# Optimization experiments

Hardware: AMD Instinct MI355X
Metric: run time of the kernel (lower is better)

The kernel has to match this reference:

```python
import jax, jax.numpy as jnp
import numpy as np

N = 100000   # nodes
E = 1600000  # edges (avg degree 16)
D_IN, D_HID, D_OUT = 128, 128, 64
BN_EPS = 1e-5


def setup_inputs() -> dict:
    key = jax.random.key(0)
    ks = jax.random.split(key, 12)
    nf_mat = jax.random.normal(ks[0], (N, D_IN), dtype=jnp.float32)
    edge_index = jax.random.randint(ks[1], (2, E), 0, N, dtype=jnp.int32)
    # pre-normalized adjacency weights (GCNConv normalize=True is folded into conv_mat here)
    edge_weight = jax.random.uniform(ks[2], (E,), dtype=jnp.float32) * (1.0 / 16.0)
    def glorot(k, fan_in, fan_out):
        s = jnp.sqrt(6.0 / (fan_in + fan_out)).astype(jnp.float32)
        return jax.random.uniform(k, (fan_in, fan_out), dtype=jnp.float32, minval=-s, maxval=s)
    return {
        "nf_mat": nf_mat,
        "edge_index": edge_index,
        "edge_weight": edge_weight,
        "W0": glorot(ks[3], D_IN, D_HID), "b0": jnp.zeros((D_HID,), jnp.float32),
        "W1": glorot(ks[4], D_HID, D_HID), "b1": jnp.zeros((D_HID,), jnp.float32),
        "W2": glorot(ks[5], D_HID, D_OUT), "b2": jnp.zeros((D_OUT,), jnp.float32),
        "gamma0": jnp.ones((D_HID,), jnp.float32), "beta0": jnp.zeros((D_HID,), jnp.float32),
        "gamma1": jnp.ones((D_HID,), jnp.float32), "beta1": jnp.zeros((D_HID,), jnp.float32),
    }


def _gcn_conv(x, W, b, src, dst, w):
    # GCNConv: aggregate A_norm @ (x W) + b over the sparse edge list
    h = x @ W                                   # [N, F_out]
    msg = h[src] * w[:, None]                   # [E, F_out] gather + scale
    agg = jax.ops.segment_sum(msg, dst, num_segments=N)  # scatter-add -> [N, F_out]
    return agg + b


def _batchnorm(x, gamma, beta):
    # BatchNorm1d over node dimension (training-mode batch statistics, biased var)
    mu = jnp.mean(x, axis=0)
    var = jnp.mean(jnp.square(x - mu), axis=0)
    return gamma * (x - mu) * jax.lax.rsqrt(var + BN_EPS) + beta


def reference(nf_mat, edge_index, edge_weight, W0, b0, W1, b1, W2, b2,
              gamma0, beta0, gamma1, beta1):
    src, dst = edge_index[0], edge_index[1]
    x = nf_mat
    # layer 0: conv -> BN -> ReLU (dropout is identity in eval)
    x = _gcn_conv(x, W0, b0, src, dst, edge_weight)
    x = jax.nn.relu(_batchnorm(x, gamma0, beta0))
    # layer 1
    x = _gcn_conv(x, W1, b1, src, dst, edge_weight)
    x = jax.nn.relu(_batchnorm(x, gamma1, beta1))
    # final conv, then cross-node sum
    x = _gcn_conv(x, W2, b2, src, dst, edge_weight)
    return jnp.sum(x, axis=0)  # [D_OUT]
```

## Files before the change

kernel.cpp:

```cpp
#include <hip/hip_runtime.h>

#define BN_EPS 1e-5f

#define NPB 512
#define NPB_SHIFT 9
#define PB 512
#define MAXB 256
#define WCB 200
#define WCCAP 16
#define NSLICE 16

typedef __attribute__((ext_vector_type(8))) short short8;
typedef __attribute__((ext_vector_type(4))) float floatx4;
typedef __attribute__((ext_vector_type(2))) float floatx2;

__device__ __forceinline__ unsigned short f2bf(float f) {
    unsigned u = __float_as_uint(f);
    unsigned r = u + 0x7FFFu + ((u >> 16) & 1u);
    return (unsigned short)(r >> 16);
}
__device__ __forceinline__ float blo(unsigned v) { return __uint_as_float(v << 16); }
__device__ __forceinline__ float bhi(unsigned v) { return __uint_as_float(v & 0xffff0000u); }

__device__ __forceinline__ uint2 pk8_fp8(const float4 v0, const float4 v1) {
    int lo = 0, hi = 0;
    lo = __builtin_amdgcn_cvt_pk_fp8_f32(v0.x, v0.y, lo, false);
    lo = __builtin_amdgcn_cvt_pk_fp8_f32(v0.z, v0.w, lo, true);
    hi = __builtin_amdgcn_cvt_pk_fp8_f32(v1.x, v1.y, hi, false);
    hi = __builtin_amdgcn_cvt_pk_fp8_f32(v1.z, v1.w, hi, true);
    return make_uint2((unsigned)lo, (unsigned)hi);
}

__global__ __launch_bounds__(256) void wconv(
    const float* __restrict__ W0, const float* __restrict__ W1,
    unsigned short* __restrict__ wt0, unsigned short* __restrict__ wt1,
    float* __restrict__ stats)
{
    const int idx = blockIdx.x * 256 + threadIdx.x;
    const int n = idx >> 7, k = idx & 127;
    wt0[idx] = f2bf(W0[k * 128 + n]);
    wt1[idx] = f2bf(W1[k * 128 + n]);
    if (blockIdx.x < 10) {
        const int o = (blockIdx.x * 256 + threadIdx.x) * 4;
        *(float4*)&stats[o] = make_float4(0.f, 0.f, 0.f, 0.f);
    }
}

__global__ __launch_bounds__(256) void gemm0(
    const float* __restrict__ A, const unsigned short* __restrict__ Wt,
    uint2* __restrict__ C, int M)
{
    __shared__ char lds[53248];
    unsigned short* Al = (unsigned short*)lds;
    unsigned short* Wl = (unsigned short*)(lds + 17408);
    float* Cl = (float*)lds;

    const int tid = threadIdx.x;
    const int r0 = blockIdx.x * 64;

#pragma unroll
    for (int i = 0; i < 16; ++i) {
        const int idx = i * 256 + tid;
        const int n = idx >> 5, q = idx & 31;
        const ushort4 v = ((const ushort4*)Wt)[idx];
        *(ushort4*)&Wl[n * 136 + q * 4] = v;
    }
#pragma unroll
    for (int i = 0; i < 8; ++i) {
        const int row = i * 8 + (tid >> 5), q = tid & 31;
        const int gr = r0 + row;
        float4 v = (gr < M) ? ((const float4*)A)[(size_t)gr * 32 + q]
                            : make_float4(0.f, 0.f, 0.f, 0.f);
        ushort4 o;
        o.x = f2bf(v.x); o.y = f2bf(v.y); o.z = f2bf(v.z); o.w = f2bf(v.w);
        *(ushort4*)&Al[row * 136 + q * 4] = o;
    }
    __syncthreads();

    const int wave = tid >> 6, lane = tid & 63;
    const int lrow = lane & 15, quad = lane >> 4;
    const int n0 = wave * 32;

    floatx4 acc[4][2];
#pragma unroll
    for (int mt = 0; mt < 4; ++mt)
#pragma unroll
        for (int t = 0; t < 2; ++t)
#pragma unroll
            for (int j = 0; j < 4; ++j) acc[mt][t][j] = 0.f;

#pragma unroll
    for (int c = 0; c < 4; ++c) {
        const int k0 = c * 32;
        const short8 b0 = *(const short8*)&Wl[(n0 + lrow) * 136 + k0 + quad * 8];
        const short8 b1 = *(const short8*)&Wl[(n0 + 16 + lrow) * 136 + k0 + quad * 8];
#pragma unroll
        for (int mt = 0; mt < 4; ++mt) {
            const short8 a = *(const short8*)&Al[(mt * 16 + lrow) * 136 + k0 + quad * 8];
            acc[mt][0] = __builtin_amdgcn_mfma_f32_16x16x32_bf16(a, b0, acc[mt][0], 0, 0, 0);
            acc[mt][1] = __builtin_amdgcn_mfma_f32_16x16x32_bf16(a, b1, acc[mt][1], 0, 0, 0);
        }
    }
    __syncthreads();

#pragma unroll
    for (int mt = 0; mt < 4; ++mt)
#pragma unroll
        for (int t = 0; t < 2; ++t)
#pragma unroll
            for (int j = 0; j < 4; ++j)
                Cl[(mt * 16 + quad * 4 + j) * 132 + n0 + t * 16 + lrow] = acc[mt][t][j];
    __syncthreads();

#pragma unroll
    for (int i = 0; i < 4; ++i) {
        const int row = i * 16 + (tid >> 4);
        const int c0 = (tid & 15) * 8;
        const int gr = r0 + row;
        if (gr < M) {
            const float4 v0 = *(float4*)&Cl[row * 132 + c0];
            const float4 v1 = *(float4*)&Cl[row * 132 + c0 + 4];
            C[(size_t)gr * 16 + (c0 >> 3)] = pk8_fp8(v0, v1);
        }
    }
}

__global__ __launch_bounds__(256) void gemm1(
    const unsigned* __restrict__ Ab, const unsigned short* __restrict__ Wt,
    uint2* __restrict__ C,
    const float* __restrict__ sum, const float* __restrict__ sq,
    const float* __restrict__ g, const float* __restrict__ be,
    int M, int N)
{
    __shared__ char lds[53248];
    unsigned short* Al = (unsigned short*)lds;
    unsigned short* Wl = (unsigned short*)(lds + 17408);
    float* AscL = (float*)(lds + 52224);
    float* AshL = AscL + 128;
    float* Cl = (float*)lds;

    const int tid = threadIdx.x;
    const int r0 = blockIdx.x * 64;

    if (tid < 128) {
        float s = 0.f, q = 0.f;
#pragma unroll
        for (int k = 0; k < NSLICE; ++k) {
            s += sum[k * 128 + tid];
            q += sq[k * 128 + tid];
        }
        const float invN = 1.0f / (float)N;
        const float m = s * invN;
        const float var = q * invN - m * m;
        const float rs = rsqrtf(var + BN_EPS);
        AscL[tid] = g[tid] * rs;
        AshL[tid] = be[tid] - g[tid] * m * rs;
    }
    __syncthreads();

#pragma unroll
    for (int i = 0; i < 16; ++i) {
        const int idx = i * 256 + tid;
        const int n = idx >> 5, q = idx & 31;
        const ushort4 v = ((const ushort4*)Wt)[idx];
        *(ushort4*)&Wl[n * 136 + q * 4] = v;
    }
#pragma unroll
    for (int i = 0; i < 4; ++i) {
        const int idx = i * 256 + tid;
        const int row = idx >> 4, qc = idx & 15;
        const int gr = r0 + row;
        uint4 v = (gr < M) ? ((const uint4*)Ab)[(size_t)gr * 16 + qc]
                           : make_uint4(0, 0, 0, 0);
        const float4 a0 = *(const float4*)&AscL[qc * 8];
        const float4 a1 = *(const float4*)&AscL[qc * 8 + 4];
        const float4 b0 = *(const float4*)&AshL[qc * 8];
        const float4 b1 = *(const float4*)&AshL[qc * 8 + 4];
        float x0 = fmaxf(fmaf(a0.x, blo(v.x), b0.x), 0.f);
        float x1 = fmaxf(fmaf(a0.y, bhi(v.x), b0.y), 0.f);
        float x2 = fmaxf(fmaf(a0.z, blo(v.y), b0.z), 0.f);
        float x3 = fmaxf(fmaf(a0.w, bhi(v.y), b0.w), 0.f);
        float x4 = fmaxf(fmaf(a1.x, blo(v.z), b1.x), 0.f);
        float x5 = fmaxf(fmaf(a1.y, bhi(v.z), b1.y), 0.f);
        float x6 = fmaxf(fmaf(a1.z, blo(v.w), b1.z), 0.f);
        float x7 = fmaxf(fmaf(a1.w, bhi(v.w), b1.w), 0.f);
        uint4 o;
        o.x = (unsigned)f2bf(x0) | ((unsigned)f2bf(x1) << 16);
        o.y = (unsigned)f2bf(x2) | ((unsigned)f2bf(x3) << 16);
        o.z = (unsigned)f2bf(x4) | ((unsigned)f2bf(x5) << 16);
        o.w = (unsigned)f2bf(x6) | ((unsigned)f2bf(x7) << 16);
        *(uint4*)&Al[row * 136 + qc * 8] = o;
    }
    __syncthreads();

    const int wave = tid >> 6, lane = tid & 63;
    const int lrow = lane & 15, quad = lane >> 4;
    const int n0 = wave * 32;

    floatx4 acc[4][2];
#pragma unroll
    for (int mt = 0; mt < 4; ++mt)
#pragma unroll
        for (int t = 0; t < 2; ++t)
#pragma unroll
            for (int j = 0; j < 4; ++j) acc[mt][t][j] = 0.f;

#pragma unroll
    for (int c = 0; c < 4; ++c) {
        const int k0 = c * 32;
        const short8 b0 = *(const short8*)&Wl[(n0 + lrow) * 136 + k0 + quad * 8];
        const short8 b1 = *(const short8*)&Wl[(n0 + 16 + lrow) * 136 + k0 + quad * 8];
#pragma unroll
        for (int mt = 0; mt < 4; ++mt) {
            const short8 a = *(const short8*)&Al[(mt * 16 + lrow) * 136 + k0 + quad * 8];
            acc[mt][0] = __builtin_amdgcn_mfma_f32_16x16x32_bf16(a, b0, acc[mt][0], 0, 0, 0);
            acc[mt][1] = __builtin_amdgcn_mfma_f32_16x16x32_bf16(a, b1, acc[mt][1], 0, 0, 0);
        }
    }
    __syncthreads();

#pragma unroll
    for (int mt = 0; mt < 4; ++mt)
#pragma unroll
        for (int t = 0; t < 2; ++t)
#pragma unroll
            for (int j = 0; j < 4; ++j)
                Cl[(mt * 16 + quad * 4 + j) * 132 + n0 + t * 16 + lrow] = acc[mt][t][j];
    __syncthreads();

#pragma unroll
    for (int i = 0; i < 4; ++i) {
        const int row = i * 16 + (tid >> 4);
        const int c0 = (tid & 15) * 8;
        const int gr = r0 + row;
        if (gr < M) {
            const float4 v0 = *(float4*)&Cl[row * 132 + c0];
            const float4 v1 = *(float4*)&Cl[row * 132 + c0 + 4];
            C[(size_t)gr * 16 + (c0 >> 3)] = pk8_fp8(v0, v1);
        }
    }
}


__global__ __launch_bounds__(512) void bucket_hist(
    const int* __restrict__ src, const int* __restrict__ dst,
    int* __restrict__ cntD, int* __restrict__ cntS, int E, int B, int chunk)
{
    __shared__ int hD[MAXB], hS[MAXB];
    const int tid = threadIdx.x;
    for (int i = tid; i < B; i += 512) { hD[i] = 0; hS[i] = 0; }
    __syncthreads();
    const int lo = blockIdx.x * chunk;
    const int hi = min(E, lo + chunk);
    for (int e = lo + tid; e < hi; e += 512) {
        atomicAdd(&hD[dst[e] >> NPB_SHIFT], 1);
        atomicAdd(&hS[src[e] >> NPB_SHIFT], 1);
    }
    __syncthreads();
    for (int i = tid; i < B; i += 512) {
        cntD[i * PB + blockIdx.x] = hD[i];
        cntS[i * PB + blockIdx.x] = hS[i];
    }
}

__global__ __launch_bounds__(256) void bucket_base(
    const int* __restrict__ cntD, const int* __restrict__ cntS,
    int* __restrict__ baseD, int* __restrict__ baseS, int B, int E)
{
    __shared__ int lD[256], lS[256];
    const int tid = threadIdx.x;
    int sD = 0, sS = 0;
    if (tid < B) {
        const int4* pD = (const int4*)(cntD + tid * PB);
        const int4* pS = (const int4*)(cntS + tid * PB);
        for (int j = 0; j < PB / 4; ++j) {
            const int4 a = pD[j], b = pS[j];
            sD += a.x + a.y + a.z + a.w;
            sS += b.x + b.y + b.z + b.w;
        }
    }
    lD[tid] = sD; lS[tid] = sS;
    __syncthreads();
    for (int st = 1; st < 256; st <<= 1) {
        const int vD = (tid >= st) ? lD[tid - st] : 0;
        const int vS = (tid >= st) ? lS[tid - st] : 0;
        __syncthreads();
        lD[tid] += vD; lS[tid] += vS;
        __syncthreads();
    }
    if (tid < B) { baseD[tid] = lD[tid] - sD; baseS[tid] = lS[tid] - sS; }
    if (tid == 0) { baseD[B] = E; baseS[B] = E; }
}

__global__ __launch_bounds__(256) void bucket_cursor(
    int* __restrict__ cntD, int* __restrict__ cntS,
    const int* __restrict__ baseD, const int* __restrict__ baseS, int B)
{
    int b = blockIdx.x;
    int* cnt; const int* base;
    if (b < B) { cnt = cntD; base = baseD; }
    else       { cnt = cntS; base = baseS; b -= B; }
    __shared__ int ls[256];
    const int tid = threadIdx.x;
    const int c0 = cnt[b * PB + 2 * tid];
    const int c1 = cnt[b * PB + 2 * tid + 1];
    const int s = c0 + c1;
    ls[tid] = s;
    __syncthreads();
    for (int st = 1; st < 256; st <<= 1) {
        const int v = (tid >= st) ? ls[tid - st] : 0;
        __syncthreads();
        ls[tid] += v;
        __syncthreads();
    }
    const int excl = ls[tid] - s + base[b];
    cnt[b * PB + 2 * tid] = excl;
    cnt[b * PB + 2 * tid + 1] = excl + c0;
}

__global__ __launch_bounds__(512) void bucket_place(
    const int* __restrict__ src, const int* __restrict__ dst,
    const float* __restrict__ ew,
    const int* __restrict__ curD, const int* __restrict__ curS,
    uint2* __restrict__ bktD, uint2* __restrict__ bktS, int E, int B, int chunk)
{
    __shared__ uint2 bufD[WCB][WCCAP + 1], bufS[WCB][WCCAP + 1];
    __shared__ int tailD[WCB], tailS[WCB], gcurD[WCB], gcurS[WCB];
    const int tid = threadIdx.x;
    for (int i = tid; i < B; i += 512) {
        gcurD[i] = curD[i * PB + blockIdx.x];
        gcurS[i] = curS[i * PB + blockIdx.x];
        tailD[i] = 0; tailS[i] = 0;
    }
    __syncthreads();
    const int lo = blockIdx.x * chunk;
    const int hi = min(E, lo + chunk);
    const int nt = (hi - lo + 511) >> 9;
    for (int t = 0; t < nt; ++t) {
        const int e = lo + t * 512 + tid;
        if (e < hi) {
            const int s = src[e], d = dst[e];
            const unsigned wb = __float_as_uint(ew[e]);
            const int bd = d >> NPB_SHIFT;
            const uint2 rd = make_uint2(((unsigned)s << NPB_SHIFT) | (unsigned)(d & (NPB - 1)), wb);
            const int pd = atomicAdd(&tailD[bd], 1);
            if (pd < WCCAP) bufD[bd][pd] = rd;
            else            bktD[gcurD[bd] + pd] = rd;
            const int bs = s >> NPB_SHIFT;
            const uint2 rs = make_uint2((unsigned)(s & (NPB - 1)), wb);
            const int ps = atomicAdd(&tailS[bs], 1);
            if (ps < WCCAP) bufS[bs][ps] = rs;
            else            bktS[gcurS[bs] + ps] = rs;
        }
        __syncthreads();
        const bool last = (t == nt - 1);
        if (tid < B) {
            {
                const int tl = tailD[tid];
                const int nb = min(tl, WCCAP);
                const int k = last ? nb : (nb & ~7);
                const int base = gcurD[tid];
                for (int i = 0; i < k; ++i) bktD[base + i] = bufD[tid][i];
                const int adv = (tl > WCCAP) ? tl : k;
                const int left = (tl > WCCAP) ? 0 : (tl - k);
                for (int i = 0; i < left; ++i) bufD[tid][i] = bufD[tid][k + i];
                gcurD[tid] = base + adv;
                tailD[tid] = left;
            }
            {
                const int tl = tailS[tid];
                const int nb = min(tl, WCCAP);
                const int k = last ? nb : (nb & ~7);
                const int base = gcurS[tid];
                for (int i = 0; i < k; ++i) bktS[base + i] = bufS[tid][i];
                const int adv = (tl > WCCAP) ? tl : k;
                const int left = (tl > WCCAP) ? 0 : (tl - k);
                for (int i = 0; i < left; ++i) bufS[tid][i] = bufS[tid][k + i];
                gcurS[tid] = base + adv;
                tailS[tid] = left;
            }
        }
        __syncthreads();
    }
}

__global__ __launch_bounds__(256) void bucket_sortcw(
    const uint2* __restrict__ bktD, const int* __restrict__ baseD,
    int* __restrict__ rp, int2* __restrict__ packed,
    const uint2* __restrict__ bktS, const int* __restrict__ baseS,
    float* __restrict__ cw, int N, int B)
{
    const int tid = threadIdx.x;
    if (blockIdx.x >= B) {
        const int b = blockIdx.x - B;
        const int lo = baseS[b], hi = baseS[b + 1];
        __shared__ float sm[NPB];
        sm[2 * tid] = 0.f; sm[2 * tid + 1] = 0.f;
        __syncthreads();
        for (int i = lo + tid; i < hi; i += 256) {
            const uint2 r = bktS[i];
            atomicAdd(&sm[r.x], __uint_as_float(r.y));
        }
        __syncthreads();
        const int n0 = b * NPB + 2 * tid;
        if (n0 < N)     cw[n0]     = sm[2 * tid];
        if (n0 + 1 < N) cw[n0 + 1] = sm[2 * tid + 1];
        return;
    }
    const int b = blockIdx.x;
    const int lo = baseD[b], hi = baseD[b + 1];
    __shared__ int cnt[NPB], cur[NPB];
    __shared__ int ls[256];
    cnt[2 * tid] = 0; cnt[2 * tid + 1] = 0;
    __syncthreads();
    for (int i = lo + tid; i < hi; i += 256)
        atomicAdd(&cnt[bktD[i].x & (NPB - 1)], 1);
    __syncthreads();
    const int c0 = cnt[2 * tid], c1 = cnt[2 * tid + 1];
    const int s = c0 + c1;
    ls[tid] = s;
    __syncthreads();
    for (int st = 1; st < 256; st <<= 1) {
        const int v = (tid >= st) ? ls[tid - st] : 0;
        __syncthreads();
        ls[tid] += v;
        __syncthreads();
    }
    const int excl = ls[tid] - s;
    const int n0 = b * NPB + 2 * tid;
    if (n0 < N)     rp[n0]     = lo + excl + c0;
    if (n0 + 1 < N) rp[n0 + 1] = lo + excl + c0 + c1;
    cur[2 * tid]     = lo + excl;
    cur[2 * tid + 1] = lo + excl + c0;
    __syncthreads();
    for (int i = lo + tid; i < hi; i += 256) {
        const uint2 r = bktD[i];
        const int pos = atomicAdd(&cur[r.x & (NPB - 1)], 1);
        packed[pos] = make_int2((int)(r.x >> NPB_SHIFT) << 4, (int)r.y);
    }
}


#define ACC_EDGE(V, W, A) do { \
    floatx2 w2_; w2_.x = (W); w2_.y = (W); \
    floatx2 f_; \
    f_ = __builtin_amdgcn_cvt_pk_f32_fp8((int)(V).x, false); \
    A[0] = f_ * w2_ + A[0]; \
    f_ = __builtin_amdgcn_cvt_pk_f32_fp8((int)(V).x, true);  \
    A[1] = f_ * w2_ + A[1]; \
    f_ = __builtin_amdgcn_cvt_pk_f32_fp8((int)(V).y, false); \
    A[2] = f_ * w2_ + A[2]; \
    f_ = __builtin_amdgcn_cvt_pk_f32_fp8((int)(V).y, true);  \
    A[3] = f_ * w2_ + A[3]; \
} while (0)

__global__ __launch_bounds__(256) void aggq(
    const int2* __restrict__ packed, const int* __restrict__ rp,
    const uint2* __restrict__ h2, uint4* __restrict__ aggb4,
    float* __restrict__ sum, float* __restrict__ sq, int N)
{
    __shared__ int2 eb[16][65];
    __shared__ float lsum[512], lsq[512];

    const int tid = threadIdx.x;
    const int lane = tid & 63, wave = tid >> 6;
    const int sub = lane >> 4;
    const int u = lane & 15;
    const int wq = wave * 4 + sub;
    const int nb0 = blockIdx.x * 32;
    const int nX = nb0 + wq * 2, nY = nX + 1;
    int2* ebq = eb[wq];

    int rpv = 0;
    {
        const int idx = nb0 - 1 + lane;
        if (lane <= 32 && idx >= 0 && idx < N) rpv = rp[idx];
    }
    const int sX = __shfl(rpv, 2 * wq, 64);
    const int eX = __shfl(rpv, 2 * wq + 1, 64);
    const int eYr = __shfl(rpv, 2 * wq + 2, 64);
    const int sY = eX;
    const int dXf = max(eX - sX, 0), dYf = max(eYr - sY, 0);
    const int eXe = sX + dXf, eYe = sY + dYf;

    {
        int2 r;
        r = (u      < dXf) ? packed[sX + u]      : make_int2(0, 0); ebq[u]      = r;
        r = (u + 16 < dXf) ? packed[sX + 16 + u] : make_int2(0, 0); ebq[16 + u] = r;
        r = (u      < dYf) ? packed[sY + u]      : make_int2(0, 0); ebq[32 + u] = r;
        r = (u + 16 < dYf) ? packed[sY + 16 + u] : make_int2(0, 0); ebq[48 + u] = r;
    }

    floatx2 aX[4], aY[4];
#pragma unroll
    for (int k = 0; k < 4; ++k) { aX[k] = 0.f; aY[k] = 0.f; }

    const int cX = min(dXf, 32), cY = min(dYf, 32);
    const int jmax = (cX > cY) ? cX : cY;

    for (int j = 0; j < jmax; j += 4) {
        const int2 x0 = ebq[j],      x1 = ebq[j + 1];
        const int2 x2 = ebq[j + 2],  x3 = ebq[j + 3];
        const int2 y0 = ebq[32 + j],     y1 = ebq[32 + j + 1];
        const int2 y2 = ebq[32 + j + 2], y3 = ebq[32 + j + 3];
        const uint2 vx0 = h2[(size_t)(unsigned)(x0.x + u)];
        const uint2 vx1 = h2[(size_t)(unsigned)(x1.x + u)];
        const uint2 vx2 = h2[(size_t)(unsigned)(x2.x + u)];
        const uint2 vx3 = h2[(size_t)(unsigned)(x3.x + u)];
        const uint2 vy0 = h2[(size_t)(unsigned)(y0.x + u)];
        const uint2 vy1 = h2[(size_t)(unsigned)(y1.x + u)];
        const uint2 vy2 = h2[(size_t)(unsigned)(y2.x + u)];
        const uint2 vy3 = h2[(size_t)(unsigned)(y3.x + u)];
        ACC_EDGE(vx0, __int_as_float(x0.y), aX);
        ACC_EDGE(vx1, __int_as_float(x1.y), aX);
        ACC_EDGE(vx2, __int_as_float(x2.y), aX);
        ACC_EDGE(vx3, __int_as_float(x3.y), aX);
        ACC_EDGE(vy0, __int_as_float(y0.y), aY);
        ACC_EDGE(vy1, __int_as_float(y1.y), aY);
        ACC_EDGE(vy2, __int_as_float(y2.y), aY);
        ACC_EDGE(vy3, __int_as_float(y3.y), aY);
    }

    for (int base = sX + 32; base < eXe; base += 32) {
        const int rem = eXe - base;
        int2 r;
        r = (u      < rem) ? packed[base + u]      : make_int2(0, 0); ebq[u]      = r;
        r = (u + 16 < rem) ? packed[base + 16 + u] : make_int2(0, 0); ebq[16 + u] = r;
        const int cc = min(rem, 32);
        for (int j = 0; j < cc; j += 4) {
            const int2 x0 = ebq[j], x1 = ebq[j + 1], x2 = ebq[j + 2], x3 = ebq[j + 3];
            const uint2 v0 = h2[(size_t)(unsigned)(x0.x + u)];
            const uint2 v1 = h2[(size_t)(unsigned)(x1.x + u)];
            const uint2 v2 = h2[(size_t)(unsigned)(x2.x + u)];
            const uint2 v3 = h2[(size_t)(unsigned)(x3.x + u)];
            ACC_EDGE(v0, __int_as_float(x0.y), aX);
            ACC_EDGE(v1, __int_as_float(x1.y), aX);
            ACC_EDGE(v2, __int_as_float(x2.y), aX);
            ACC_EDGE(v3, __int_as_float(x3.y), aX);
        }
    }
    for (int base = sY + 32; base < eYe; base += 32) {
        const int rem = eYe - base;
        int2 r;
        r = (u      < rem) ? packed[base + u]      : make_int2(0, 0); ebq[32 + u] = r;
        r = (u + 16 < rem) ? packed[base + 16 + u] : make_int2(0, 0); ebq[48 + u] = r;
        const int cc = min(rem, 32);
        for (int j = 0; j < cc; j += 4) {
            const int2 y0 = ebq[32 + j], y1 = ebq[32 + j + 1];
            const int2 y2 = ebq[32 + j + 2], y3 = ebq[32 + j + 3];
            const uint2 v0 = h2[(size_t)(unsigned)(y0.x + u)];
            const uint2 v1 = h2[(size_t)(unsigned)(y1.x + u)];
            const uint2 v2 = h2[(size_t)(unsigned)(y2.x + u)];
            const uint2 v3 = h2[(size_t)(unsigned)(y3.x + u)];
            ACC_EDGE(v0, __int_as_float(y0.y), aY);
            ACC_EDGE(v1, __int_as_float(y1.y), aY);
            ACC_EDGE(v2, __int_as_float(y2.y), aY);
            ACC_EDGE(v3, __int_as_float(y3.y), aY);
        }
    }

    if (nX < N) {
        uint4 o;
        o.x = (unsigned)f2bf(aX[0].x) | ((unsigned)f2bf(aX[0].y) << 16);
        o.y = (unsigned)f2bf(aX[1].x) | ((unsigned)f2bf(aX[1].y) << 16);
        o.z = (unsigned)f2bf(aX[2].x) | ((unsigned)f2bf(aX[2].y) << 16);
        o.w = (unsigned)f2bf(aX[3].x) | ((unsigned)f2bf(aX[3].y) << 16);
        aggb4[(size_t)nX * 16 + u] = o;
    }
    if (nY < N) {
        uint4 o;
        o.x = (unsigned)f2bf(aY[0].x) | ((unsigned)f2bf(aY[0].y) << 16);
        o.y = (unsigned)f2bf(aY[1].x) | ((unsigned)f2bf(aY[1].y) << 16);
        o.z = (unsigned)f2bf(aY[2].x) | ((unsigned)f2bf(aY[2].y) << 16);
        o.w = (unsigned)f2bf(aY[3].x) | ((unsigned)f2bf(aY[3].y) << 16);
        aggb4[(size_t)nY * 16 + u] = o;
    }

    floatx2 cs0 = aX[0] + aY[0], cs1 = aX[1] + aY[1];
    floatx2 cs2 = aX[2] + aY[2], cs3 = aX[3] + aY[3];
    floatx2 cq0 = aX[0] * aX[0] + aY[0] * aY[0];
    floatx2 cq1 = aX[1] * aX[1] + aY[1] * aY[1];
    floatx2 cq2 = aX[2] * aX[2] + aY[2] * aY[2];
    floatx2 cq3 = aX[3] * aX[3] + aY[3] * aY[3];
#define XRED(V) \
    V.x += __shfl_xor(V.x, 16, 64); V.y += __shfl_xor(V.y, 16, 64); \
    V.x += __shfl_xor(V.x, 32, 64); V.y += __shfl_xor(V.y, 32, 64);
    XRED(cs0) XRED(cs1) XRED(cs2) XRED(cs3)
    XRED(cq0) XRED(cq1) XRED(cq2) XRED(cq3)
#undef XRED
    const floatx2 ws = (sub == 0) ? cs0 : (sub == 1) ? cs1 : (sub == 2) ? cs2 : cs3;
    const floatx2 wwq = (sub == 0) ? cq0 : (sub == 1) ? cq1 : (sub == 2) ? cq2 : cq3;
    const int col = u * 8 + 2 * sub;
    lsum[wave * 128 + col] = ws.x;  lsum[wave * 128 + col + 1] = ws.y;
    lsq[wave * 128 + col]  = wwq.x; lsq[wave * 128 + col + 1]  = wwq.y;
    __syncthreads();
    if (tid < 128) {
        float s = 0.f, q = 0.f;
#pragma unroll
        for (int i = 0; i < 4; ++i) {
            s += lsum[i * 128 + tid];
            q += lsq[i * 128 + tid];
        }
        const int sl = (blockIdx.x & (NSLICE - 1)) * 128;
        atomicAdd(&sum[sl + tid], s);
        atomicAdd(&sq[sl + tid], q);
    }
}

__global__ __launch_bounds__(256) void wcolsum_bf16(
    const uint2* __restrict__ xb2, const float* __restrict__ cw,
    const float* __restrict__ sum1, const float* __restrict__ sq1,
    const float* __restrict__ g, const float* __restrict__ be,
    float* __restrict__ sout, int N)
{
    __shared__ float Aaf[128], Baf[128];
    __shared__ float4 ls[256];
    const int tid = threadIdx.x;
    if (tid < 128) {
        float s = 0.f, q = 0.f;
#pragma unroll
        for (int k = 0; k < NSLICE; ++k) {
            s += sum1[k * 128 + tid];
            q += sq1[k * 128 + tid];
        }
        const float invN = 1.0f / (float)N;
        const float m = s * invN;
        const float var = q * invN - m * m;
        const float rs = rsqrtf(var + BN_EPS);
        Aaf[tid] = g[tid] * rs;
        Baf[tid] = be[tid] - g[tid] * m * rs;
    }
    __syncthreads();
    const int u2 = tid & 31;
    const int half = (tid >> 5) & 1;
    const int rr = tid >> 6;
    const float4 A = *(const float4*)&Aaf[u2 * 4];
    const float4 Bv = *(const float4*)&Baf[u2 * 4];
    float4 s = make_float4(0.f, 0.f, 0.f, 0.f);
    for (int row = blockIdx.x * 8 + rr * 2 + half; row < N; row += gridDim.x * 8) {
        const uint2 v = xb2[(size_t)row * 32 + u2];
        const float c = cw[row];
        s.x = fmaf(c, fmaxf(fmaf(A.x, blo(v.x), Bv.x), 0.f), s.x);
        s.y = fmaf(c, fmaxf(fmaf(A.y, bhi(v.x), Bv.y), 0.f), s.y);
        s.z = fmaf(c, fmaxf(fmaf(A.z, blo(v.y), Bv.z), 0.f), s.z);
        s.w = fmaf(c, fmaxf(fmaf(A.w, bhi(v.y), Bv.w), 0.f), s.w);
    }
    ls[tid] = s;
    __syncthreads();
    if (tid < 32) {
        float4 a = ls[tid];
#pragma unroll
        for (int k = 1; k < 8; ++k) {
            const float4 b = ls[tid + 32 * k];
            a.x += b.x; a.y += b.y; a.z += b.z; a.w += b.w;
        }
        float* so = sout + (blockIdx.x & (NSLICE - 1)) * 128 + tid * 4;
        atomicAdd(&so[0], a.x);
        atomicAdd(&so[1], a.y);
        atomicAdd(&so[2], a.z);
        atomicAdd(&so[3], a.w);
    }
}

__global__ void final_out(
    const float* __restrict__ s, const float* __restrict__ W2,
    const float* __restrict__ b2, float* __restrict__ out, int N, int Dout)
{
    __shared__ float sv[128];
    const int j = threadIdx.x;
    {
        float a = 0.f;
#pragma unroll
        for (int k = 0; k < NSLICE; ++k) a += s[k * 128 + j];
        sv[j] = a;
    }
    __syncthreads();
    if (j < Dout) {
        float acc = 0.f;
        for (int f = 0; f < 128; ++f) acc = fmaf(sv[f], W2[f * Dout + j], acc);
        out[j] = acc + (float)N * b2[j];
    }
}

extern "C" void kernel_launch(void* const* d_in, const int* in_sizes, int n_in,
                              void* d_out, int out_size, void* d_ws, size_t ws_size,
                              hipStream_t stream)
{
    const float* nf  = (const float*)d_in[0];
    const int*   ei  = (const int*)d_in[1];
    const float* ew  = (const float*)d_in[2];
    const float* W0  = (const float*)d_in[3];
    const float* W1  = (const float*)d_in[5];
    const float* W2  = (const float*)d_in[7];
    const float* b2  = (const float*)d_in[8];
    const float* g0  = (const float*)d_in[9];
    const float* be0 = (const float*)d_in[10];
    const float* g1  = (const float*)d_in[11];
    const float* be1 = (const float*)d_in[12];

    const int N = in_sizes[0] / 128;
    const int E = in_sizes[2];
    const int* srcI = ei;
    const int* dstI = ei + E;

    const int B = (N + NPB - 1) / NPB;
    const int chunk = (E + PB - 1) / PB;

    const size_t HB = ((size_t)N * 128 * 2 + 255) & ~(size_t)255;
    const size_t NA = ((size_t)N * sizeof(int) + 255) & ~(size_t)255;
    const size_t CB = (((size_t)B * PB * 4) + 255) & ~(size_t)255;
    char* ws = (char*)d_ws;
    size_t off = 0;
    float* cw    = (float*)(ws + off); off += NA;
    int*   rp    = (int*)  (ws + off); off += NA;
    float* stats = (float*)(ws + off); off += 40960;
    int*   cntD  = (int*)  (ws + off); off += CB;
    int*   cntS  = (int*)  (ws + off); off += CB;
    int*   baseD = (int*)  (ws + off); off += 2048;
    int*   baseS = (int*)  (ws + off); off += 2048;
    uint2* hbuf  = (uint2*)(ws + off); off += HB;
    unsigned* aggb = (unsigned*)(ws + off); off += HB;
    int2*  packed = (int2*)(ws + off); off += (size_t)E * 8;
    uint2* bktD  = (uint2*)(ws + off); off += (size_t)E * 8;
    uint2* bktS  = (uint2*)(ws + off); off += (size_t)E * 8;
    unsigned short* wt0 = (unsigned short*)(ws + off); off += 32768;
    unsigned short* wt1 = (unsigned short*)(ws + off); off += 32768;
    (void)ws_size;

    float* sum0 = stats + 0 * NSLICE * 128;
    float* sq0  = stats + 1 * NSLICE * 128;
    float* sum1 = stats + 2 * NSLICE * 128;
    float* sq1  = stats + 3 * NSLICE * 128;
    float* svec = stats + 4 * NSLICE * 128;

    const int gemmGrid = (N + 63) / 64;
    const int aggGrid  = (N + 31) / 32;

    bucket_hist<<<PB, 512, 0, stream>>>(srcI, dstI, cntD, cntS, E, B, chunk);
    bucket_base<<<1, 256, 0, stream>>>(cntD, cntS, baseD, baseS, B, E);
    bucket_cursor<<<2 * B, 256, 0, stream>>>(cntD, cntS, baseD, baseS, B);
    bucket_place<<<PB, 512, 0, stream>>>(srcI, dstI, ew, cntD, cntS, bktD, bktS, E, B, chunk);
    bucket_sortcw<<<2 * B, 256, 0, stream>>>(bktD, baseD, rp, packed,
                                             bktS, baseS, cw, N, B);
    wconv<<<64, 256, 0, stream>>>(W0, W1, wt0, wt1, stats);

    gemm0<<<gemmGrid, 256, 0, stream>>>(nf, wt0, hbuf, N);
    aggq<<<aggGrid, 256, 0, stream>>>(
        packed, rp, (const uint2*)hbuf, (uint4*)aggb, sum0, sq0, N);

    gemm1<<<gemmGrid, 256, 0, stream>>>(aggb, wt1, hbuf, sum0, sq0, g0, be0, N, N);
    aggq<<<aggGrid, 256, 0, stream>>>(
        packed, rp, (const uint2*)hbuf, (uint4*)aggb, sum1, sq1, N);

    wcolsum_bf16<<<2048, 256, 0, stream>>>((const uint2*)aggb, cw, sum1, sq1,
                                           g1, be1, svec, N);
    final_out<<<1, 128, 0, stream>>>(svec, W2, b2, (float*)d_out, N, out_size);
}
```

Baseline: 335.7 us.

## Parallelize bucket flush, stage per-bucket sort in LDS, widen aggregation unroll

The per-bucket write-combine flush in bucket_place is now spread across all threads instead of one thread per bucket looping serially. bucket_sortcw moves to 512 threads with one node per thread, and it builds the sorted CSR segment in shared memory before writing it out coalesced. Buckets larger than SCAP still use direct scattered writes. The first-tile loop in aggq now issues 8 gathers per stream instead of 4 for more memory-level parallelism, at the cost of more registers and one extra barrier per flush.

```diff
diff --git a/kernel.cpp b/kernel.cpp
--- a/kernel.cpp
+++ b/kernel.cpp
@@ -8,6 +8,7 @@
 #define MAXB 256
 #define WCB 200
 #define WCCAP 16
+#define SCAP 10240
 #define NSLICE 16
 
 typedef __attribute__((ext_vector_type(8))) short short8;
@@ -326,6 +327,7 @@
 {
     __shared__ uint2 bufD[WCB][WCCAP + 1], bufS[WCB][WCCAP + 1];
     __shared__ int tailD[WCB], tailS[WCB], gcurD[WCB], gcurS[WCB];
+    __shared__ int kD[WCB], kS[WCB], bD[WCB], bS[WCB];
     const int tid = threadIdx.x;
     for (int i = tid; i < B; i += 512) {
         gcurD[i] = curD[i * PB + blockIdx.x];
@@ -355,36 +357,43 @@
         __syncthreads();
         const bool last = (t == nt - 1);
         if (tid < B) {
+            int tl = tailD[tid];
+            int nb = min(tl, WCCAP);
+            kD[tid] = last ? nb : (nb & ~7);
+            bD[tid] = gcurD[tid];
+            tl = tailS[tid];
+            nb = min(tl, WCCAP);
+            kS[tid] = last ? nb : (nb & ~7);
+            bS[tid] = gcurS[tid];
+        }
+        __syncthreads();
+        for (int x = tid; x < B * WCCAP; x += 512) {
+            const int bb = x >> 4, i = x & (WCCAP - 1);
+            if (i < kD[bb]) bktD[bD[bb] + i] = bufD[bb][i];
+            if (i < kS[bb]) bktS[bS[bb] + i] = bufS[bb][i];
+        }
+        __syncthreads();
+        if (tid < B) {
             {
-                const int tl = tailD[tid];
-                const int nb = min(tl, WCCAP);
-                const int k = last ? nb : (nb & ~7);
-                const int base = gcurD[tid];
-                for (int i = 0; i < k; ++i) bktD[base + i] = bufD[tid][i];
+                const int tl = tailD[tid], k = kD[tid];
                 const int adv = (tl > WCCAP) ? tl : k;
                 const int left = (tl > WCCAP) ? 0 : (tl - k);
                 for (int i = 0; i < left; ++i) bufD[tid][i] = bufD[tid][k + i];
-                gcurD[tid] = base + adv;
-                tailD[tid] = left;
+                gcurD[tid] += adv; tailD[tid] = left;
             }
             {
-                const int tl = tailS[tid];
-                const int nb = min(tl, WCCAP);
-                const int k = last ? nb : (nb & ~7);
-                const int base = gcurS[tid];
-                for (int i = 0; i < k; ++i) bktS[base + i] = bufS[tid][i];
+                const int tl = tailS[tid], k = kS[tid];
                 const int adv = (tl > WCCAP) ? tl : k;
                 const int left = (tl > WCCAP) ? 0 : (tl - k);
                 for (int i = 0; i < left; ++i) bufS[tid][i] = bufS[tid][k + i];
-                gcurS[tid] = base + adv;
-                tailS[tid] = left;
+                gcurS[tid] += adv; tailS[tid] = left;
             }
         }
         __syncthreads();
     }
 }
 
-__global__ __launch_bounds__(256) void bucket_sortcw(
+__global__ __launch_bounds__(512) void bucket_sortcw(
     const uint2* __restrict__ bktD, const int* __restrict__ baseD,
     int* __restrict__ rp, int2* __restrict__ packed,
     const uint2* __restrict__ bktS, const int* __restrict__ baseS,
@@ -395,48 +404,60 @@
         const int b = blockIdx.x - B;
         const int lo = baseS[b], hi = baseS[b + 1];
         __shared__ float sm[NPB];
-        sm[2 * tid] = 0.f; sm[2 * tid + 1] = 0.f;
-        __syncthreads();
-        for (int i = lo + tid; i < hi; i += 256) {
+        sm[tid] = 0.f;
+        __syncthreads();
+        for (int i = lo + tid; i < hi; i += 512) {
             const uint2 r = bktS[i];
             atomicAdd(&sm[r.x], __uint_as_float(r.y));
         }
         __syncthreads();
-        const int n0 = b * NPB + 2 * tid;
-        if (n0 < N)     cw[n0]     = sm[2 * tid];
-        if (n0 + 1 < N) cw[n0 + 1] = sm[2 * tid + 1];
+        const int n0 = b * NPB + tid;
+        if (n0 < N) cw[n0] = sm[tid];
         return;
     }
     const int b = blockIdx.x;
     const int lo = baseD[b], hi = baseD[b + 1];
+    const int sz = hi - lo;
     __shared__ int cnt[NPB], cur[NPB];
-    __shared__ int ls[256];
-    cnt[2 * tid] = 0; cnt[2 * tid + 1] = 0;
-    __syncthreads();
-    for (int i = lo + tid; i < hi; i += 256)
+    __shared__ int2 stage[SCAP];
+    cnt[tid] = 0;
+    __syncthreads();
+    for (int i = lo + tid; i < hi; i += 512)
         atomicAdd(&cnt[bktD[i].x & (NPB - 1)], 1);
     __syncthreads();
-    const int c0 = cnt[2 * tid], c1 = cnt[2 * tid + 1];
-    const int s = c0 + c1;
-    ls[tid] = s;
-    __syncthreads();
-    for (int st = 1; st < 256; st <<= 1) {
+    int* ls = (int*)stage;
+    const int c = cnt[tid];
+    ls[tid] = c;
+    __syncthreads();
+    for (int st = 1; st < NPB; st <<= 1) {
         const int v = (tid >= st) ? ls[tid - st] : 0;
         __syncthreads();
         ls[tid] += v;
         __syncthreads();
     }
-    const int excl = ls[tid] - s;
-    const int n0 = b * NPB + 2 * tid;
-    if (n0 < N)     rp[n0]     = lo + excl + c0;
-    if (n0 + 1 < N) rp[n0 + 1] = lo + excl + c0 + c1;
-    cur[2 * tid]     = lo + excl;
-    cur[2 * tid + 1] = lo + excl + c0;
-    __syncthreads();
-    for (int i = lo + tid; i < hi; i += 256) {
-        const uint2 r = bktD[i];
-        const int pos = atomicAdd(&cur[r.x & (NPB - 1)], 1);
-        packed[pos] = make_int2((int)(r.x >> NPB_SHIFT) << 4, (int)r.y);
+    const int incl = ls[tid];
+    __syncthreads();
+    {
+        const int n0 = b * NPB + tid;
+        if (n0 < N) rp[n0] = lo + incl;
+        cur[tid] = incl - c;
+    }
+    __syncthreads();
+    if (sz <= SCAP) {
+        for (int i = lo + tid; i < hi; i += 512) {
+            const uint2 r = bktD[i];
+            const int pos = atomicAdd(&cur[r.x & (NPB - 1)], 1);
+            stage[pos] = make_int2((int)(r.x >> NPB_SHIFT) << 4, (int)r.y);
+        }
+        __syncthreads();
+        for (int i = tid; i < sz; i += 512)
+            packed[lo + i] = stage[i];
+    } else {
+        for (int i = lo + tid; i < hi; i += 512) {
+            const uint2 r = bktD[i];
+            const int pos = atomicAdd(&cur[r.x & (NPB - 1)], 1);
+            packed[lo + pos] = make_int2((int)(r.x >> NPB_SHIFT) << 4, (int)r.y);
+        }
     }
 }
 
@@ -498,27 +519,19 @@
     const int cX = min(dXf, 32), cY = min(dYf, 32);
     const int jmax = (cX > cY) ? cX : cY;
 
-    for (int j = 0; j < jmax; j += 4) {
-        const int2 x0 = ebq[j],      x1 = ebq[j + 1];
-        const int2 x2 = ebq[j + 2],  x3 = ebq[j + 3];
-        const int2 y0 = ebq[32 + j],     y1 = ebq[32 + j + 1];
-        const int2 y2 = ebq[32 + j + 2], y3 = ebq[32 + j + 3];
-        const uint2 vx0 = h2[(size_t)(unsigned)(x0.x + u)];
-        const uint2 vx1 = h2[(size_t)(unsigned)(x1.x + u)];
-        const uint2 vx2 = h2[(size_t)(unsigned)(x2.x + u)];
-        const uint2 vx3 = h2[(size_t)(unsigned)(x3.x + u)];
-        const uint2 vy0 = h2[(size_t)(unsigned)(y0.x + u)];
-        const uint2 vy1 = h2[(size_t)(unsigned)(y1.x + u)];
-        const uint2 vy2 = h2[(size_t)(unsigned)(y2.x + u)];
-        const uint2 vy3 = h2[(size_t)(unsigned)(y3.x + u)];
-        ACC_EDGE(vx0, __int_as_float(x0.y), aX);
-        ACC_EDGE(vx1, __int_as_float(x1.y), aX);
-        ACC_EDGE(vx2, __int_as_float(x2.y), aX);
-        ACC_EDGE(vx3, __int_as_float(x3.y), aX);
-        ACC_EDGE(vy0, __int_as_float(y0.y), aY);
-        ACC_EDGE(vy1, __int_as_float(y1.y), aY);
-        ACC_EDGE(vy2, __int_as_float(y2.y), aY);
-        ACC_EDGE(vy3, __int_as_float(y3.y), aY);
+    for (int j = 0; j < jmax; j += 8) {
+        int2 x[8], y[8];
+#pragma unroll
+        for (int t = 0; t < 8; ++t) { x[t] = ebq[j + t]; y[t] = ebq[32 + j + t]; }
+        uint2 vx[8], vy[8];
+#pragma unroll
+        for (int t = 0; t < 8; ++t) vx[t] = h2[(size_t)(unsigned)(x[t].x + u)];
+#pragma unroll
+        for (int t = 0; t < 8; ++t) vy[t] = h2[(size_t)(unsigned)(y[t].x + u)];
+#pragma unroll
+        for (int t = 0; t < 8; ++t) ACC_EDGE(vx[t], __int_as_float(x[t].y), aX);
+#pragma unroll
+        for (int t = 0; t < 8; ++t) ACC_EDGE(vy[t], __int_as_float(y[t].y), aY);
     }
 
     for (int base = sX + 32; base < eXe; base += 32) {
@@ -740,7 +753,7 @@
     bucket_base<<<1, 256, 0, stream>>>(cntD, cntS, baseD, baseS, B, E);
     bucket_cursor<<<2 * B, 256, 0, stream>>>(cntD, cntS, baseD, baseS, B);
     bucket_place<<<PB, 512, 0, stream>>>(srcI, dstI, ew, cntD, cntS, bktD, bktS, E, B, chunk);
-    bucket_sortcw<<<2 * B, 256, 0, stream>>>(bktD, baseD, rp, packed,
+    bucket_sortcw<<<2 * B, 512, 0, stream>>>(bktD, baseD, rp, packed,
                                              bktS, baseS, cw, N, B);
     wconv<<<64, 256, 0, stream>>>(W0, W1, wt0, wt1, stats);
 
```

Result: no change. 342.0 us (+1.9%).
